# Kernel optimization log

Hardware: AMD Instinct MI355X
Metric: run time of the kernel (lower is better)

The kernel has to match this reference:

```python
import jax, jax.numpy as jnp
import numpy as np

NUM_HEADS = 8
DIM_HEAD_QK = 32
DIM_HEAD_V = 32
BLOCK = 8
HALO = 3
WIN = BLOCK + 2 * HALO  # 14
SCALE = DIM_HEAD_QK ** -0.5


def rel_logits_1d(q, rel_k, permute_mask):
    N, H, W, d = q.shape
    rel_size = rel_k.shape[0]
    win = (rel_size + 1) // 2
    x = jnp.einsum('nhwd,rd->nhwr', q, rel_k)
    x = x.reshape(N * H, W, rel_size)
    x = jnp.pad(x, ((0, 0), (0, 0), (0, 1))).reshape(N * H, -1)
    x = jnp.pad(x, ((0, 0), (0, rel_size - W)))
    x = x.reshape(N * H, W + 1, rel_size)[:, :W, win - 1:]
    x = jnp.broadcast_to(x.reshape(N, H, 1, W, win), (N, H, win, W, win))
    return jnp.transpose(x, permute_mask)


def pos_embed_rel(q, height_rel, width_rel):
    BH, NB, HW, d = q.shape
    qb = q.reshape(-1, BLOCK, BLOCK, d)
    rel_w = rel_logits_1d(qb, width_rel, (0, 1, 3, 2, 4))
    rel_h = rel_logits_1d(jnp.swapaxes(qb, 1, 2), height_rel, (0, 3, 1, 4, 2))
    return (rel_h + rel_w).reshape(BH, NB, HW, WIN * WIN)


def reference(x, q_weight, kv_weight, height_rel, width_rel):
    B, C, H, W = x.shape
    nhb, nwb = H // BLOCK, W // BLOCK
    nb = nhb * nwb
    # 1x1 conv projections
    q = jnp.einsum('bchw,oc->bohw', x, q_weight)
    q = q.reshape(B * NUM_HEADS, DIM_HEAD_QK, nhb, BLOCK, nwb, BLOCK)
    q = jnp.transpose(q, (0, 1, 3, 5, 2, 4)).reshape(B * NUM_HEADS, DIM_HEAD_QK, BLOCK * BLOCK, nb)
    q = jnp.swapaxes(q, 1, 3)  # (BH, nb, BLOCK*BLOCK, dhq)
    kv = jnp.einsum('bchw,oc->bohw', x, kv_weight)
    kv = jnp.pad(kv, ((0, 0), (0, 0), (HALO, HALO), (HALO, HALO)))
    # halo windows: overlapping WINxWIN patches strided by BLOCK
    h_idx = jnp.arange(nhb)[:, None] * BLOCK + jnp.arange(WIN)[None, :]
    w_idx = jnp.arange(nwb)[:, None] * BLOCK + jnp.arange(WIN)[None, :]
    kv = kv[:, :, h_idx, :][:, :, :, :, w_idx]
    kv = jnp.transpose(kv, (0, 1, 2, 4, 3, 5)).reshape(
        B * NUM_HEADS, DIM_HEAD_QK + DIM_HEAD_V, nb, WIN * WIN)
    kv = jnp.transpose(kv, (0, 2, 3, 1))
    k, v = kv[..., :DIM_HEAD_QK], kv[..., DIM_HEAD_QK:]
    attn = jnp.einsum('bnqd,bnkd->bnqk', q, k) * SCALE
    attn = attn + pos_embed_rel(q, height_rel, width_rel)
    attn = jax.nn.softmax(attn, axis=-1)
    out = jnp.einsum('bnqk,bnkd->bnqd', attn, v)
    out = jnp.swapaxes(out, 1, 3)  # (BH, dhv, BLOCK*BLOCK, nb)
    out = out.reshape(-1, BLOCK, BLOCK, nhb, nwb)
    out = jnp.transpose(out, (0, 3, 1, 4, 2)).reshape(B, NUM_HEADS * DIM_HEAD_V, H, W)
    return out


def setup_inputs() -> dict:
    key = jax.random.key(0)
    k1, k2, k3, k4, k5 = jax.random.split(key, 5)
    dim = 256
    std = dim ** -0.5
    x = jax.random.normal(k1, (8, 256, 96, 96), dtype=jnp.float32)
    q_weight = jax.random.normal(k2, (256, 256), dtype=jnp.float32) * std
    kv_weight = jax.random.normal(k3, (512, 256), dtype=jnp.float32) * std
    height_rel = jax.random.normal(k4, (2 * WIN - 1, DIM_HEAD_QK), dtype=jnp.float32) * SCALE
    width_rel = jax.random.normal(k5, (2 * WIN - 1, DIM_HEAD_QK), dtype=jnp.float32) * SCALE
    return {'x': x, 'q_weight': q_weight, 'kv_weight': kv_weight,
            'height_rel': height_rel, 'width_rel': width_rel}
```

## Files before the change

### kernel.cpp

```cpp
#include <hip/hip_runtime.h>
#include <math.h>

#define NPIX 9216
#define SCALE 0.17677669529663687f
#define LOG2E 1.4426950408889634f
#define PSL   (SCALE * LOG2E)
#define RINV  5.656854249492381f

typedef __attribute__((ext_vector_type(8))) short bh8;
typedef __attribute__((ext_vector_type(4))) float f4;

__device__ __forceinline__ unsigned short f2bf(float f) {
    unsigned u = __float_as_uint(f);
    u += 0x7fff + ((u >> 16) & 1);
    return (unsigned short)(u >> 16);
}
__device__ __forceinline__ void gload_lds16(const void* g, void* l) {
    __builtin_amdgcn_global_load_lds(
        (const __attribute__((address_space(1))) unsigned int*)g,
        (__attribute__((address_space(3))) unsigned int*)l, 16, 0, 0);
}

__global__ void wconv_kernel(const float* __restrict__ qw, const float* __restrict__ kvw,
                             const float* __restrict__ hrel, const float* __restrict__ wrel,
                             unsigned short* __restrict__ Wb,
                             unsigned short* __restrict__ relb) {
    int bid = blockIdx.x, tid = threadIdx.x;
    if (bid < 768) {
        float v = (bid < 256) ? qw[bid * 256 + tid] : kvw[(bid - 256) * 256 + tid];
        Wb[bid * 256 + tid] = f2bf(v);
    } else {
        int e = (bid - 768) * 256 + tid;
        int half = e >> 10, r = (e >> 5) & 31, d = e & 31;
        float v = 0.0f;
        if (r < 27) v = (half ? wrel : hrel)[r * 32 + d] * RINV;
        relb[half * 1024 + r * 32 + d] = f2bf(v);
    }
}

__global__ __launch_bounds__(256) void xtrans_kernel(const float* __restrict__ x,
                                                     unsigned short* __restrict__ xt) {
    int b = blockIdx.z;
    int p0 = blockIdx.x * 128, c0 = blockIdx.y * 128;
    int tid = threadIdx.x;
    __shared__ __align__(16) unsigned short ts[128 * 128];
    const float* xb = x + (size_t)b * 256 * NPIX;
    #pragma unroll
    for (int it = 0; it < 16; ++it) {
        int e = it * 256 + tid;
        int ch = e >> 5, p4 = (e & 31) * 4;
        float4 v = *(const float4*)(xb + (size_t)(c0 + ch) * NPIX + p0 + p4);
        int sw = ((p4 >> 3) & 7) << 4;
        char* tb = (char*)ts;
        *(unsigned short*)(tb + (((p4 + 0) * 256 + ch * 2) ^ sw)) = f2bf(v.x);
        *(unsigned short*)(tb + (((p4 + 1) * 256 + ch * 2) ^ sw)) = f2bf(v.y);
        *(unsigned short*)(tb + (((p4 + 2) * 256 + ch * 2) ^ sw)) = f2bf(v.z);
        *(unsigned short*)(tb + (((p4 + 3) * 256 + ch * 2) ^ sw)) = f2bf(v.w);
    }
    __syncthreads();
    unsigned short* xtb = xt + (size_t)b * NPIX * 256;
    #pragma unroll
    for (int it = 0; it < 8; ++it) {
        int e = it * 256 + tid;
        int p = e >> 4, ck = (e & 15) * 8;
        int bo = (p * 256 + ck * 2) ^ (((p >> 3) & 7) << 4);
        *(int4*)(xtb + (size_t)(p0 + p) * 256 + c0 + ck) = *(const int4*)((char*)ts + bo);
    }
}

__global__ __launch_bounds__(256) void proj_kernel(const unsigned short* __restrict__ xt,
                                                   const unsigned short* __restrict__ Wb,
                                                   unsigned short* __restrict__ qb,
                                                   unsigned short* __restrict__ kvb) {
    int flat = blockIdx.x + 72 * (blockIdx.y + 6 * blockIdx.z);
    int w = (flat & 7) * 432 + (flat >> 3);
    int n0 = (w % 6) * 128;
    int m0 = ((w / 6) % 72) * 128;
    int b  = w / 432;
    int tid = threadIdx.x, lane = tid & 63, wave = tid >> 6;
    int ll = lane & 15;
    __shared__ __align__(16) char smem[34816];
    char* As = smem;
    char* Bs = smem + 16384;
    const unsigned short* xtb = xt + (size_t)b * NPIX * 256;

    f4 acc[4][4] = {};
    int wm = (wave & 1) * 64, wn = (wave >> 1) * 64;

    for (int k0 = 0; k0 < 256; k0 += 64) {
        __syncthreads();
        #pragma unroll
        for (int i = 0; i < 4; ++i) {
            int c = wave * 4 + i;
            gload_lds16(xtb + (size_t)(m0 + c * 8 + (lane >> 3)) * 256 + k0 + (lane & 7) * 8,
                        As + c * 1024);
            gload_lds16(Wb + (size_t)(n0 + c * 8 + (lane >> 3)) * 256 + k0 + (lane & 7) * 8,
                        Bs + c * 1024);
        }
        __syncthreads();
        #pragma unroll
        for (int ks = 0; ks < 2; ++ks) {
            bh8 af[4], bf[4];
            #pragma unroll
            for (int i = 0; i < 4; ++i)
                af[i] = *(const bh8*)(As + (wm + i * 16 + ll) * 128 + ks * 64 + (lane >> 4) * 16);
            #pragma unroll
            for (int j = 0; j < 4; ++j)
                bf[j] = *(const bh8*)(Bs + (wn + j * 16 + ll) * 128 + ks * 64 + (lane >> 4) * 16);
            #pragma unroll
            for (int i = 0; i < 4; ++i)
                #pragma unroll
                for (int j = 0; j < 4; ++j)
                    acc[i][j] = __builtin_amdgcn_mfma_f32_16x16x32_bf16(af[i], bf[j], acc[i][j], 0, 0, 0);
        }
    }

    __syncthreads();
    unsigned short* ts = (unsigned short*)smem;
    bool isQ = (n0 < 256);
    float osc = isQ ? PSL : 1.0f;
    int q4 = (lane >> 4) * 4;
    #pragma unroll
    for (int i = 0; i < 4; ++i) {
        #pragma unroll
        for (int j = 0; j < 4; ++j) {
            int ch = wn + j * 16 + ll;
            #pragma unroll
            for (int r = 0; r < 4; ++r)
                ts[(wm + i * 16 + q4 + r) * 136 + ch] = f2bf(acc[i][j][r] * osc);
        }
    }
    __syncthreads();
    #pragma unroll
    for (int it = 0; it < 8; ++it) {
        int e = it * 256 + tid;
        int pixl = e >> 4, ck = (e & 15) * 8;
        int4 v = *(const int4*)&ts[pixl * 136 + ck];
        int pix = m0 + pixl, ch = n0 + ck;
        if (isQ) {
            int head = ch >> 5, d = ch & 31;
            *(int4*)&qb[((size_t)(b * 8 + head) * NPIX + pix) * 32 + d] = v;
        } else {
            int c = ch - 256, head = c >> 6, dv = c & 63;
            *(int4*)&kvb[((size_t)(b * 8 + head) * NPIX + pix) * 64 + dv] = v;
        }
    }
}

__global__ __launch_bounds__(256, 4) void attn_kernel(const unsigned short* __restrict__ qbuf,
                                                      const unsigned short* __restrict__ kvbuf,
                                                      const unsigned short* __restrict__ relb,
                                                      float* __restrict__ out) {
    int flat = blockIdx.x + 144 * blockIdx.y;
    int w = (flat & 7) * 1152 + (flat >> 3);
    int nbid = w % 144, bh = w / 144;
    int b = bh >> 3, head = bh & 7;
    int hb = nbid / 12, wblk = nbid % 12;
    int r0 = hb * 8, c0 = wblk * 8;
    int tid = threadIdx.x, lane = tid & 63, wave = tid >> 6;
    int ll = lane & 15, lq = lane >> 4;
    int m0 = wave * 16;

    __shared__ __align__(16) char smem[32512];
    unsigned short* Vt = (unsigned short*)smem;
    unsigned short* Ks = (unsigned short*)(smem + 14336);
    char* strip = smem + 14336 + wave * 4352;
    float*          RhTw = (float*)strip;
    float*          Rww  = (float*)(strip + 2240);
    unsigned short* Ps   = (unsigned short*)strip;
    float*          smR  = (float*)(smem + 32256);

    const unsigned short* qb  = qbuf  + (size_t)bh * NPIX * 32;
    const unsigned short* kvb = kvbuf + (size_t)bh * NPIX * 64;

    int qp0 = m0 + ll;
    int pixq = (r0 + (qp0 >> 3)) * 96 + c0 + (qp0 & 7);
    bh8 aq = *(const bh8*)&qb[(size_t)pixq * 32 + lq * 8];

    for (int e = tid; e < 896; e += 256) {
        int kp = e >> 2, part = e & 3;
        int a = kp >> 4, b2 = kp & 15;
        int gr = r0 + a - 3, gc = c0 + b2 - 3;
        int4 v = {0, 0, 0, 0};
        if (b2 < 14 && (unsigned)gr < 96u && (unsigned)gc < 96u)
            v = *(const int4*)&kvb[(size_t)(gr * 96 + gc) * 64 + part * 8];
        *(int4*)&Ks[kp * 40 + part * 8] = v;
    }

    #pragma unroll
    for (int it = 0; it < 2; ++it) {
        int e = it * 256 + tid;
        int part = e >> 7, kp2 = e & 127;
        if (kp2 < 112) {
            int a = kp2 >> 3, b2 = (kp2 & 7) * 2;
            int gr = r0 + a - 3, gc = c0 + b2 - 3;
            int4 lo = {0, 0, 0, 0}, hi = {0, 0, 0, 0};
            bool rok = ((kp2 & 7) < 7) && ((unsigned)gr < 96u);
            if (rok && (unsigned)gc < 96u)
                lo = *(const int4*)&kvb[(size_t)(gr * 96 + gc) * 64 + 32 + part * 8];
            if (rok && (unsigned)(gc + 1) < 96u)
                hi = *(const int4*)&kvb[(size_t)(gr * 96 + gc + 1) * 64 + 32 + part * 8];
            int g = kp2 >> 2, kb = b2 & 7;
            const unsigned* lw = (const unsigned*)&lo;
            const unsigned* hw = (const unsigned*)&hi;
            #pragma unroll
            for (int jw = 0; jw < 4; ++jw) {
                unsigned l2 = lw[jw], h2 = hw[jw];
                unsigned v0 = (l2 & 0xffffu) | (h2 << 16);
                unsigned v1 = (l2 >> 16) | (h2 & 0xffff0000u);
                int d0 = part * 8 + jw * 2;
                int s0 = (((jw * 2) & 3) + part) & 3;
                int s1 = (((jw * 2 + 1) & 3) + part) & 3;
                *(unsigned*)&Vt[d0 * 224 + ((g ^ s0) * 8) + kb] = v0;
                *(unsigned*)&Vt[(d0 + 1) * 224 + ((g ^ s1) * 8) + kb] = v1;
            }
        }
    }

    __syncthreads();

    f4 zero4 = {0.f, 0.f, 0.f, 0.f};
    f4 S[14];
    #pragma unroll
    for (int t = 0; t < 14; ++t) {
        bh8 bk = *(const bh8*)&Ks[(t * 16 + ll) * 40 + lq * 8];
        S[t] = __builtin_amdgcn_mfma_f32_16x16x32_bf16(aq, bk, zero4, 0, 0, 0);
    }

    __syncthreads();

    #pragma unroll
    for (int t = 0; t < 2; ++t) {
        int r = t * 16 + ll;
        bh8 hbv = *(const bh8*)&relb[(size_t)r * 32 + lq * 8];
        bh8 wbv = *(const bh8*)&relb[1024 + (size_t)r * 32 + lq * 8];
        f4 ch = __builtin_amdgcn_mfma_f32_16x16x32_bf16(aq, hbv, zero4, 0, 0, 0);
        f4 cw = __builtin_amdgcn_mfma_f32_16x16x32_bf16(aq, wbv, zero4, 0, 0, 0);
        if (r < 28) *(f4*)&RhTw[r * 20 + lq * 4] = ch;
        if (r >= 6 && r < 27) {
            #pragma unroll
            for (int rr = 0; rr < 4; ++rr)
                Rww[(lq * 4 + rr) * 23 + (r - 6)] = cw[rr];
        }
    }

    int row0 = m0 + lq * 4;
    int h = row0 >> 3;
    bool valid = (ll < 14);
    float rw4[4];
    #pragma unroll
    for (int rr = 0; rr < 4; ++rr) {
        int row = row0 + rr;
        rw4[rr] = valid ? Rww[(lq * 4 + rr) * 23 + 7 + ll - (row & 7)] : -INFINITY;
    }
    float sm4[4] = {0.f, 0.f, 0.f, 0.f};
    #pragma unroll
    for (int t = 0; t < 14; ++t) {
        f4 rh = *(const f4*)&RhTw[(13 + t - h) * 20 + lq * 4];
        #pragma unroll
        for (int rr = 0; rr < 4; ++rr) {
            float lg = (S[t][rr] + rh[rr]) + rw4[rr];
            float p = __builtin_amdgcn_exp2f(lg);
            S[t][rr] = p;
            sm4[rr] += p;
        }
    }
    #pragma unroll
    for (int rr = 0; rr < 4; ++rr) {
        sm4[rr] += __shfl_xor(sm4[rr], 1);
        sm4[rr] += __shfl_xor(sm4[rr], 2);
        sm4[rr] += __shfl_xor(sm4[rr], 4);
        sm4[rr] += __shfl_xor(sm4[rr], 8);
    }
    if (ll == 0) {
        #pragma unroll
        for (int rr = 0; rr < 4; ++rr) smR[row0 + rr] = sm4[rr];
    }

    int sel = ll & 1;
    int rowA = lq * 4 + sel * 2;
    f4 O[2] = {zero4, zero4};
    #pragma unroll
    for (int c = 0; c < 2; ++c) {
        const int nt = c ? 6 : 8;
        #pragma unroll
        for (int tl = 0; tl < 8; ++tl) {
            if (tl < nt) {
                int t = c * 8 + tl;
                float o0 = S[t][0], o1 = S[t][1], o2 = S[t][2], o3 = S[t][3];
                float q0 = __shfl_xor(o0, 1), q1 = __shfl_xor(o1, 1);
                float q2 = __shfl_xor(o2, 1), q3 = __shfl_xor(o3, 1);
                float lo0 = sel ? q2 : o0, hi0 = sel ? o2 : q0;
                float lo1 = sel ? q3 : o1, hi1 = sel ? o3 : q1;
                unsigned w0, w1;
                asm("v_cvt_pk_bf16_f32 %0, %1, %2" : "=v"(w0) : "v"(lo0), "v"(hi0));
                asm("v_cvt_pk_bf16_f32 %0, %1, %2" : "=v"(w1) : "v"(lo1), "v"(hi1));
                int colp = tl * 16 + (ll & ~1);
                *(unsigned*)&Ps[rowA * 136 + colp]       = w0;
                *(unsigned*)&Ps[(rowA + 1) * 136 + colp] = w1;
            }
        }
        const int nkt = c ? 3 : 4;
        #pragma unroll
        for (int ktl = 0; ktl < 4; ++ktl) {
            if (ktl < nkt) {
                int kt = c * 4 + ktl;
                bh8 bp = *(const bh8*)&Ps[ll * 136 + ktl * 32 + lq * 8];
                #pragma unroll
                for (int mt = 0; mt < 2; ++mt) {
                    int d = mt * 16 + ll;
                    int s = ((d & 3) + ((d >> 3) & 3)) & 3;
                    bh8 av = *(const bh8*)&Vt[d * 224 + (((kt * 4 + lq) ^ s) * 8)];
                    O[mt] = __builtin_amdgcn_mfma_f32_16x16x32_bf16(av, bp, O[mt], 0, 0, 0);
                }
            }
        }
    }

    int qp = m0 + ll;
    float rs = 1.0f / smR[qp];
    int pix = (r0 + (qp >> 3)) * 96 + c0 + (qp & 7);
    float* ob = out + (size_t)(b * 256 + head * 32) * NPIX;
    #pragma unroll
    for (int mt = 0; mt < 2; ++mt) {
        #pragma unroll
        for (int rr = 0; rr < 4; ++rr) {
            int d = mt * 16 + lq * 4 + rr;
            ob[(size_t)d * NPIX + pix] = O[mt][rr] * rs;
        }
    }
}

extern "C" void kernel_launch(void* const* d_in, const int* in_sizes, int n_in,
                              void* d_out, int out_size, void* d_ws, size_t ws_size,
                              hipStream_t stream) {
    const float* x    = (const float*)d_in[0];
    const float* qw   = (const float*)d_in[1];
    const float* kvw  = (const float*)d_in[2];
    const float* hrel = (const float*)d_in[3];
    const float* wrel = (const float*)d_in[4];
    float* out = (float*)d_out;

    char* ws = (char*)d_ws;
    unsigned short* xt    = (unsigned short*)ws;
    unsigned short* Wb    = (unsigned short*)(ws + 37748736);
    unsigned short* relb  = (unsigned short*)(ws + 38141952);
    unsigned short* qbuf  = (unsigned short*)(ws + 38146048);
    unsigned short* kvbuf = (unsigned short*)(ws + 75894784);

    wconv_kernel<<<dim3(776), 256, 0, stream>>>(qw, kvw, hrel, wrel, Wb, relb);
    xtrans_kernel<<<dim3(72, 2, 8), 256, 0, stream>>>(x, xt);
    proj_kernel<<<dim3(72, 6, 8), 256, 0, stream>>>(xt, Wb, qbuf, kvbuf);
    attn_kernel<<<dim3(144, 64), 256, 0, stream>>>(qbuf, kvbuf, relb, out);
}
```

Baseline: 265.9 us.

## Fuse fp32-to-bf16 transpose of x into projection GEMM A-tile load

Removes the separate xtrans kernel and its bf16 transposed workspace. The projection GEMM now reads fp32 x directly, converts channel pairs to packed bf16 and writes a swizzled A tile into LDS. This drops one launch and the write and re-read of a transposed copy of x. In exchange, each of the 6 N-tiles reloads fp32 x, doubling bytes per load versus bf16, and the A path becomes synchronous register loads instead of async global_load_lds.

```diff
diff --git a/kernel.cpp b/kernel.cpp
--- a/kernel.cpp
+++ b/kernel.cpp
@@ -38,37 +38,7 @@
     }
 }
 
-__global__ __launch_bounds__(256) void xtrans_kernel(const float* __restrict__ x,
-                                                     unsigned short* __restrict__ xt) {
-    int b = blockIdx.z;
-    int p0 = blockIdx.x * 128, c0 = blockIdx.y * 128;
-    int tid = threadIdx.x;
-    __shared__ __align__(16) unsigned short ts[128 * 128];
-    const float* xb = x + (size_t)b * 256 * NPIX;
-    #pragma unroll
-    for (int it = 0; it < 16; ++it) {
-        int e = it * 256 + tid;
-        int ch = e >> 5, p4 = (e & 31) * 4;
-        float4 v = *(const float4*)(xb + (size_t)(c0 + ch) * NPIX + p0 + p4);
-        int sw = ((p4 >> 3) & 7) << 4;
-        char* tb = (char*)ts;
-        *(unsigned short*)(tb + (((p4 + 0) * 256 + ch * 2) ^ sw)) = f2bf(v.x);
-        *(unsigned short*)(tb + (((p4 + 1) * 256 + ch * 2) ^ sw)) = f2bf(v.y);
-        *(unsigned short*)(tb + (((p4 + 2) * 256 + ch * 2) ^ sw)) = f2bf(v.z);
-        *(unsigned short*)(tb + (((p4 + 3) * 256 + ch * 2) ^ sw)) = f2bf(v.w);
-    }
-    __syncthreads();
-    unsigned short* xtb = xt + (size_t)b * NPIX * 256;
-    #pragma unroll
-    for (int it = 0; it < 8; ++it) {
-        int e = it * 256 + tid;
-        int p = e >> 4, ck = (e & 15) * 8;
-        int bo = (p * 256 + ck * 2) ^ (((p >> 3) & 7) << 4);
-        *(int4*)(xtb + (size_t)(p0 + p) * 256 + c0 + ck) = *(const int4*)((char*)ts + bo);
-    }
-}
-
-__global__ __launch_bounds__(256) void proj_kernel(const unsigned short* __restrict__ xt,
+__global__ __launch_bounds__(256) void proj_kernel(const float* __restrict__ x,
                                                    const unsigned short* __restrict__ Wb,
                                                    unsigned short* __restrict__ qb,
                                                    unsigned short* __restrict__ kvb) {
@@ -82,28 +52,51 @@
     __shared__ __align__(16) char smem[34816];
     char* As = smem;
     char* Bs = smem + 16384;
-    const unsigned short* xtb = xt + (size_t)b * NPIX * 256;
+    const float* xb = x + (size_t)b * 256 * NPIX;
 
     f4 acc[4][4] = {};
     int wm = (wave & 1) * 64, wn = (wave >> 1) * 64;
 
+    int pix8  = (tid & 15) * 8;
+    int cbase = tid >> 4;
+    unsigned wsw = (unsigned)((tid & 3) << 5);
+
     for (int k0 = 0; k0 < 256; k0 += 64) {
         __syncthreads();
         #pragma unroll
         for (int i = 0; i < 4; ++i) {
             int c = wave * 4 + i;
-            gload_lds16(xtb + (size_t)(m0 + c * 8 + (lane >> 3)) * 256 + k0 + (lane & 7) * 8,
-                        As + c * 1024);
             gload_lds16(Wb + (size_t)(n0 + c * 8 + (lane >> 3)) * 256 + k0 + (lane & 7) * 8,
                         Bs + c * 1024);
         }
+        #pragma unroll
+        for (int cc = 0; cc < 2; ++cc) {
+            int c = cbase + cc * 16;
+            const float* r0p = xb + (size_t)(k0 + 2 * c) * NPIX + m0 + pix8;
+            f4 a0 = *(const f4*)(r0p);
+            f4 a1 = *(const f4*)(r0p + 4);
+            f4 b0 = *(const f4*)(r0p + NPIX);
+            f4 b1 = *(const f4*)(r0p + NPIX + 4);
+            int rowb = pix8 * 128 + c * 4;
+            #pragma unroll
+            for (int j = 0; j < 4; ++j) {
+                unsigned w0, w1;
+                asm("v_cvt_pk_bf16_f32 %0, %1, %2" : "=v"(w0) : "v"(a0[j]), "v"(b0[j]));
+                asm("v_cvt_pk_bf16_f32 %0, %1, %2" : "=v"(w1) : "v"(a1[j]), "v"(b1[j]));
+                *(unsigned*)(As + ((rowb + j * 128) ^ wsw))       = w0;
+                *(unsigned*)(As + ((rowb + (j + 4) * 128) ^ wsw)) = w1;
+            }
+        }
         __syncthreads();
         #pragma unroll
         for (int ks = 0; ks < 2; ++ks) {
             bh8 af[4], bf[4];
             #pragma unroll
-            for (int i = 0; i < 4; ++i)
-                af[i] = *(const bh8*)(As + (wm + i * 16 + ll) * 128 + ks * 64 + (lane >> 4) * 16);
+            for (int i = 0; i < 4; ++i) {
+                int row = wm + i * 16 + ll;
+                unsigned rsw = (unsigned)(((row >> 3) & 3) << 5);
+                af[i] = *(const bh8*)(As + ((row * 128 + ks * 64 + (lane >> 4) * 16) ^ rsw));
+            }
             #pragma unroll
             for (int j = 0; j < 4; ++j)
                 bf[j] = *(const bh8*)(Bs + (wn + j * 16 + ll) * 128 + ks * 64 + (lane >> 4) * 16);
@@ -342,14 +335,12 @@
     float* out = (float*)d_out;
 
     char* ws = (char*)d_ws;
-    unsigned short* xt    = (unsigned short*)ws;
-    unsigned short* Wb    = (unsigned short*)(ws + 37748736);
-    unsigned short* relb  = (unsigned short*)(ws + 38141952);
-    unsigned short* qbuf  = (unsigned short*)(ws + 38146048);
-    unsigned short* kvbuf = (unsigned short*)(ws + 75894784);
+    unsigned short* Wb    = (unsigned short*)ws;
+    unsigned short* relb  = (unsigned short*)(ws + 393216);
+    unsigned short* qbuf  = (unsigned short*)(ws + 397312);
+    unsigned short* kvbuf = (unsigned short*)(ws + 38146048);
 
     wconv_kernel<<<dim3(776), 256, 0, stream>>>(qw, kvw, hrel, wrel, Wb, relb);
-    xtrans_kernel<<<dim3(72, 2, 8), 256, 0, stream>>>(x, xt);
-    proj_kernel<<<dim3(72, 6, 8), 256, 0, stream>>>(xt, Wb, qbuf, kvbuf);
+    proj_kernel<<<dim3(72, 6, 8), 256, 0, stream>>>(x, Wb, qbuf, kvbuf);
     attn_kernel<<<dim3(144, 64), 256, 0, stream>>>(qbuf, kvbuf, relb, out);
 }
```

Result: slower. 279.4 us (+5.1%).
